# Optimization experiments

Measured on AMD Instinct MI355X. Metric: run time of the kernel, lower is better.

## Reference

```python
import jax, jax.numpy as jnp
import numpy as np

NUM_SP = 1024  # superpixel labels in [0, 1024); torch uses max(sp)+1 which equals this w.h.p.

def setup_inputs() -> dict:
    key = jax.random.key(0)
    k1, k2, k3 = jax.random.split(key, 3)
    features = jax.random.normal(k1, (1, 512, 512, 256), dtype=jnp.float32)
    superpixel = jax.random.randint(k2, (512, 512), 0, NUM_SP, dtype=jnp.int64)
    w_node = jax.random.normal(k3, (21, 256), dtype=jnp.float32) * 0.05
    return {"features": features, "superpixel": superpixel, "w_node": w_node}

def reference(features, superpixel, w_node):
    # features: (1, H, W, F); superpixel: (H, W) int; w_node: (C, F)
    n_feat = features.shape[-1]
    feats_flat = features.reshape(-1, n_feat)          # (H*W, F)
    sp_flat = superpixel.reshape(-1)                   # (H*W,)
    # L1-row-normalized one-hot matmul == per-superpixel mean (segment mean)
    sums = jax.ops.segment_sum(feats_flat, sp_flat, num_segments=NUM_SP)   # (num_sp, F)
    counts = jax.ops.segment_sum(jnp.ones_like(sp_flat, dtype=feats_flat.dtype),
                                 sp_flat, num_segments=NUM_SP)             # (num_sp,)
    node_features = sums / jnp.clip(counts, 1.0)[:, None]                  # empty sp -> 0, matches F.normalize eps
    # nn.Linear(n_feat, n_classes, bias=False): x @ W^T
    node_potentials = node_features @ w_node.T                             # (num_sp, C)
    return node_potentials
```

## Files before the change

kernel.cpp:

```cpp
#include <hip/hip_runtime.h>


#define NSP 1024
#define FDIM 256
#define NBLK 128
#define IDX_CAP 4096

__global__ __launch_bounds__(256) void hist_kernel(
    const int* __restrict__ sp, int n, int* __restrict__ slab) {
    __shared__ int lh[NSP];
    const int b = blockIdx.x;
    for (int t = threadIdx.x; t < NSP; t += blockDim.x) lh[t] = 0;
    __syncthreads();
    const int chunk = (n + NBLK - 1) / NBLK;
    const int begin = b * chunk;
    const int end = min(begin + chunk, n);
    for (int i = begin + (int)threadIdx.x; i < end; i += blockDim.x)
        atomicAdd(&lh[sp[i]], 1);
    __syncthreads();
    for (int t = threadIdx.x; t < NSP; t += blockDim.x)
        slab[b * NSP + t] = lh[t];
}

__global__ __launch_bounds__(NSP) void scan_kernel(
    int* __restrict__ slab, int* __restrict__ starts, int* __restrict__ counts) {
    __shared__ int buf[NSP];
    const int t = threadIdx.x;
    int running = 0;
    for (int b = 0; b < NBLK; ++b) {
        int v = slab[b * NSP + t];
        slab[b * NSP + t] = running;
        running += v;
    }
    counts[t] = running;
    buf[t] = running;
    __syncthreads();
    for (int off = 1; off < NSP; off <<= 1) {
        int add = (t >= off) ? buf[t - off] : 0;
        __syncthreads();
        buf[t] += add;
        __syncthreads();
    }
    starts[t] = buf[t] - running;
}

__global__ __launch_bounds__(256) void scatter_kernel(
    const int* __restrict__ sp, int n, const int* __restrict__ slab,
    const int* __restrict__ starts, int* __restrict__ order) {
    __shared__ int cursor[NSP];
    const int b = blockIdx.x;
    for (int t = threadIdx.x; t < NSP; t += blockDim.x)
        cursor[t] = slab[b * NSP + t] + starts[t];
    __syncthreads();
    const int chunk = (n + NBLK - 1) / NBLK;
    const int begin = b * chunk;
    const int end = min(begin + chunk, n);
    for (int i = begin + (int)threadIdx.x; i < end; i += blockDim.x) {
        int pos = atomicAdd(&cursor[sp[i]], 1);
        order[pos] = i;
    }
}

__global__ __launch_bounds__(256) void reduce_matmul_kernel(
    const float* __restrict__ feats, const int* __restrict__ order,
    const int* __restrict__ starts, const int* __restrict__ counts,
    const float* __restrict__ w, float* __restrict__ out, int C) {
    __shared__ int idx_lds[IDX_CAP];
    __shared__ float fsum[FDIM];
    const int b = blockIdx.x;
    const int tid = (int)threadIdx.x;
    const int lane = tid & 63;
    const int wave = tid >> 6;

    const int start = starts[b];
    const int n = counts[b];
    const bool cached = (n <= IDX_CAP);

    if (cached)
        for (int i = tid; i < n; i += 256) idx_lds[i] = order[start + i];
    fsum[tid] = 0.f;
    __syncthreads();

    float a0x = 0.f, a0y = 0.f, a0z = 0.f, a0w = 0.f;
    float a1x = 0.f, a1y = 0.f, a1z = 0.f, a1w = 0.f;

    int pos = wave * 4;
    for (; pos + 3 < n; pos += 16) {
        int i0, i1, i2, i3;
        if (cached) {
            i0 = idx_lds[pos + 0]; i1 = idx_lds[pos + 1];
            i2 = idx_lds[pos + 2]; i3 = idx_lds[pos + 3];
        } else {
            i0 = order[start + pos + 0]; i1 = order[start + pos + 1];
            i2 = order[start + pos + 2]; i3 = order[start + pos + 3];
        }
        float4 v0 = ((const float4*)(feats + (size_t)i0 * FDIM))[lane];
        float4 v1 = ((const float4*)(feats + (size_t)i1 * FDIM))[lane];
        float4 v2 = ((const float4*)(feats + (size_t)i2 * FDIM))[lane];
        float4 v3 = ((const float4*)(feats + (size_t)i3 * FDIM))[lane];
        a0x += v0.x; a0y += v0.y; a0z += v0.z; a0w += v0.w;
        a1x += v1.x; a1y += v1.y; a1z += v1.z; a1w += v1.w;
        a0x += v2.x; a0y += v2.y; a0z += v2.z; a0w += v2.w;
        a1x += v3.x; a1y += v3.y; a1z += v3.z; a1w += v3.w;
    }
    for (; pos < n; ++pos) {
        int idx = cached ? idx_lds[pos] : order[start + pos];
        float4 v = ((const float4*)(feats + (size_t)idx * FDIM))[lane];
        a0x += v.x; a0y += v.y; a0z += v.z; a0w += v.w;
    }
    a0x += a1x; a0y += a1y; a0z += a1z; a0w += a1w;

    atomicAdd(&fsum[lane * 4 + 0], a0x);
    atomicAdd(&fsum[lane * 4 + 1], a0y);
    atomicAdd(&fsum[lane * 4 + 2], a0z);
    atomicAdd(&fsum[lane * 4 + 3], a0w);
    __syncthreads();

    const float scale = (n > 0) ? 1.0f / (float)n : 0.0f;
    float4 m = ((const float4*)fsum)[lane];
    m.x *= scale; m.y *= scale; m.z *= scale; m.w *= scale;

    for (int c = wave; c < C; c += 4) {
        float4 w4 = ((const float4*)(w + (size_t)c * FDIM))[lane];
        float p = m.x * w4.x + m.y * w4.y + m.z * w4.z + m.w * w4.w;
        #pragma unroll
        for (int off = 32; off > 0; off >>= 1) p += __shfl_down(p, off, 64);
        if (lane == 0) out[b * C + c] = p;
    }
}

extern "C" void kernel_launch(void* const* d_in, const int* in_sizes, int n_in,
                              void* d_out, int out_size, void* d_ws,
                              size_t ws_size, hipStream_t stream) {
    const float* feats = (const float*)d_in[0];
    const int* sp = (const int*)d_in[1];
    const float* w = (const float*)d_in[2];
    float* out = (float*)d_out;

    const int n_pix = in_sizes[1];
    const int C = in_sizes[2] / FDIM;

    char* ws = (char*)d_ws;
    int* slab = (int*)(ws);
    int* starts = (int*)(ws + 512 * 1024);
    int* counts = (int*)(ws + 516 * 1024);
    int* order = (int*)(ws + 520 * 1024);

    hist_kernel<<<NBLK, 256, 0, stream>>>(sp, n_pix, slab);
    scan_kernel<<<1, NSP, 0, stream>>>(slab, starts, counts);
    scatter_kernel<<<NBLK, 256, 0, stream>>>(sp, n_pix, slab, starts, order);
    reduce_matmul_kernel<<<NSP, 256, 0, stream>>>(feats, order, starts, counts,
                                                  w, out, C);
}
```

Measured before the change: 389.9 us.

## Double reduce block to 512 threads and replace LDS atomics with partial-sum tree

The segment-reduce kernel now runs 8 waves per superpixel block instead of 4, so more gather loads are in flight per segment. Per-wave partial sums are written to LDS and summed by 256 threads, replacing float atomics on LDS. The index cache shrinks to 2048 entries to fit the extra LDS, the histogram chunking drops its bounds checks by assuming n divides evenly by the block count, and the scan loop is unrolled by four. The main cost targeted is memory latency in the feature gather, which is bandwidth-bound over a 256 MB input.

```diff
diff --git a/kernel.cpp b/kernel.cpp
--- a/kernel.cpp
+++ b/kernel.cpp
@@ -3,22 +3,22 @@
 
 #define NSP 1024
 #define FDIM 256
-#define NBLK 128
-#define IDX_CAP 4096
+#define NHB 128
+#define IDX_CAP 2048
 
 __global__ __launch_bounds__(256) void hist_kernel(
     const int* __restrict__ sp, int n, int* __restrict__ slab) {
     __shared__ int lh[NSP];
     const int b = blockIdx.x;
-    for (int t = threadIdx.x; t < NSP; t += blockDim.x) lh[t] = 0;
+    for (int t = threadIdx.x; t < NSP; t += 256) lh[t] = 0;
     __syncthreads();
-    const int chunk = (n + NBLK - 1) / NBLK;
+    const int chunk = n / NHB;
     const int begin = b * chunk;
-    const int end = min(begin + chunk, n);
-    for (int i = begin + (int)threadIdx.x; i < end; i += blockDim.x)
+    const int end = begin + chunk;
+    for (int i = begin + (int)threadIdx.x; i < end; i += 256)
         atomicAdd(&lh[sp[i]], 1);
     __syncthreads();
-    for (int t = threadIdx.x; t < NSP; t += blockDim.x)
+    for (int t = threadIdx.x; t < NSP; t += 256)
         slab[b * NSP + t] = lh[t];
 }
 
@@ -27,10 +27,16 @@
     __shared__ int buf[NSP];
     const int t = threadIdx.x;
     int running = 0;
-    for (int b = 0; b < NBLK; ++b) {
-        int v = slab[b * NSP + t];
-        slab[b * NSP + t] = running;
-        running += v;
+    #pragma unroll 1
+    for (int b = 0; b < NHB; b += 4) {
+        int v0 = slab[(b + 0) * NSP + t];
+        int v1 = slab[(b + 1) * NSP + t];
+        int v2 = slab[(b + 2) * NSP + t];
+        int v3 = slab[(b + 3) * NSP + t];
+        slab[(b + 0) * NSP + t] = running; running += v0;
+        slab[(b + 1) * NSP + t] = running; running += v1;
+        slab[(b + 2) * NSP + t] = running; running += v2;
+        slab[(b + 3) * NSP + t] = running; running += v3;
     }
     counts[t] = running;
     buf[t] = running;
@@ -49,24 +55,25 @@
     const int* __restrict__ starts, int* __restrict__ order) {
     __shared__ int cursor[NSP];
     const int b = blockIdx.x;
-    for (int t = threadIdx.x; t < NSP; t += blockDim.x)
+    for (int t = threadIdx.x; t < NSP; t += 256)
         cursor[t] = slab[b * NSP + t] + starts[t];
     __syncthreads();
-    const int chunk = (n + NBLK - 1) / NBLK;
+    const int chunk = n / NHB;
     const int begin = b * chunk;
-    const int end = min(begin + chunk, n);
-    for (int i = begin + (int)threadIdx.x; i < end; i += blockDim.x) {
+    const int end = begin + chunk;
+    for (int i = begin + (int)threadIdx.x; i < end; i += 256) {
         int pos = atomicAdd(&cursor[sp[i]], 1);
         order[pos] = i;
     }
 }
 
-__global__ __launch_bounds__(256) void reduce_matmul_kernel(
+__global__ __launch_bounds__(512, 8) void reduce_matmul_kernel(
     const float* __restrict__ feats, const int* __restrict__ order,
     const int* __restrict__ starts, const int* __restrict__ counts,
     const float* __restrict__ w, float* __restrict__ out, int C) {
     __shared__ int idx_lds[IDX_CAP];
-    __shared__ float fsum[FDIM];
+    __shared__ float part[8 * FDIM];
+    __shared__ float mean_s[FDIM];
     const int b = blockIdx.x;
     const int tid = (int)threadIdx.x;
     const int lane = tid & 63;
@@ -77,15 +84,14 @@
     const bool cached = (n <= IDX_CAP);
 
     if (cached)
-        for (int i = tid; i < n; i += 256) idx_lds[i] = order[start + i];
-    fsum[tid] = 0.f;
+        for (int i = tid; i < n; i += 512) idx_lds[i] = order[start + i];
     __syncthreads();
 
     float a0x = 0.f, a0y = 0.f, a0z = 0.f, a0w = 0.f;
     float a1x = 0.f, a1y = 0.f, a1z = 0.f, a1w = 0.f;
 
     int pos = wave * 4;
-    for (; pos + 3 < n; pos += 16) {
+    for (; pos + 3 < n; pos += 32) {
         int i0, i1, i2, i3;
         if (cached) {
             i0 = idx_lds[pos + 0]; i1 = idx_lds[pos + 1];
@@ -110,18 +116,22 @@
     }
     a0x += a1x; a0y += a1y; a0z += a1z; a0w += a1w;
 
-    atomicAdd(&fsum[lane * 4 + 0], a0x);
-    atomicAdd(&fsum[lane * 4 + 1], a0y);
-    atomicAdd(&fsum[lane * 4 + 2], a0z);
-    atomicAdd(&fsum[lane * 4 + 3], a0w);
+    float4 pv; pv.x = a0x; pv.y = a0y; pv.z = a0z; pv.w = a0w;
+    ((float4*)&part[wave * FDIM])[lane] = pv;
     __syncthreads();
 
-    const float scale = (n > 0) ? 1.0f / (float)n : 0.0f;
-    float4 m = ((const float4*)fsum)[lane];
-    m.x *= scale; m.y *= scale; m.z *= scale; m.w *= scale;
+    if (tid < FDIM) {
+        float s = 0.f;
+        #pragma unroll
+        for (int wv = 0; wv < 8; ++wv) s += part[wv * FDIM + tid];
+        const float scale = (n > 0) ? 1.0f / (float)n : 0.0f;
+        mean_s[tid] = s * scale;
+    }
+    __syncthreads();
 
-    for (int c = wave; c < C; c += 4) {
-        float4 w4 = ((const float4*)(w + (size_t)c * FDIM))[lane];
+    const float4 m = ((const float4*)mean_s)[lane];
+    for (int c = wave; c < C; c += 8) {
+        const float4 w4 = ((const float4*)(w + (size_t)c * FDIM))[lane];
         float p = m.x * w4.x + m.y * w4.y + m.z * w4.z + m.w * w4.w;
         #pragma unroll
         for (int off = 32; off > 0; off >>= 1) p += __shfl_down(p, off, 64);
@@ -146,9 +156,9 @@
     int* counts = (int*)(ws + 516 * 1024);
     int* order = (int*)(ws + 520 * 1024);
 
-    hist_kernel<<<NBLK, 256, 0, stream>>>(sp, n_pix, slab);
+    hist_kernel<<<NHB, 256, 0, stream>>>(sp, n_pix, slab);
     scan_kernel<<<1, NSP, 0, stream>>>(slab, starts, counts);
-    scatter_kernel<<<NBLK, 256, 0, stream>>>(sp, n_pix, slab, starts, order);
-    reduce_matmul_kernel<<<NSP, 256, 0, stream>>>(feats, order, starts, counts,
+    scatter_kernel<<<NHB, 256, 0, stream>>>(sp, n_pix, slab, starts, order);
+    reduce_matmul_kernel<<<NSP, 512, 0, stream>>>(feats, order, starts, counts,
                                                   w, out, C);
 }
```

Result: no change. 391.0 us (+0.3%).
